# Kernel optimization log

Hardware: AMD Instinct MI355X
Metric: run time of the kernel (lower is better)

The kernel has to match this reference:

```python
import jax, jax.numpy as jnp
import numpy as np

B, N, IN_DIM, D, H, NC = 4, 1024, 8, 128, 8, 64
DK = D // H      # per-head key/value dim = 16
FF = 512         # hard-coded feedforward hidden
N_ENC = 6        # encoder layers


def _u(key, shape):
    s = 1.0 / np.sqrt(shape[-1])
    return jax.random.uniform(key, shape, jnp.float32, -s, s)


def setup_inputs() -> dict:
    key = jax.random.key(0)
    ks = jax.random.split(key, 24)
    inp = {}
    inp["node_inputs"] = jax.random.normal(ks[0], (B, N, IN_DIM), jnp.float32)
    inp["node_padding_mask"] = jnp.zeros((B, 1, N), jnp.int32)
    inp["edge_mask"] = jax.random.randint(ks[1], (B, N, N), 0, 2).astype(jnp.int32)
    inp["center_mask"] = jnp.zeros((B, 1, NC), jnp.int32)
    inp["center_index"] = jax.random.randint(ks[2], (B, 1, NC), 0, N)
    inp["target_index"] = jax.random.randint(ks[3], (B, 1, 1), 0, N)
    inp["current_index"] = jax.random.randint(ks[4], (B, 1, 1), 0, N)
    inp["edge_inputs"] = jax.random.randint(ks[5], (B, N, 20), 0, N)
    # params
    inp["init_W"] = _u(ks[6], (IN_DIM, D)); inp["init_b"] = jnp.zeros((D,), jnp.float32)
    inp["enc_wq"] = _u(ks[7], (N_ENC, H, D, DK))
    inp["enc_wk"] = _u(ks[8], (N_ENC, H, D, DK))
    inp["enc_wv"] = _u(ks[9], (N_ENC, H, D, DK))
    inp["enc_wo"] = _u(ks[10], (N_ENC, H, DK, D))
    inp["enc_ln1_g"] = jnp.ones((N_ENC, D), jnp.float32); inp["enc_ln1_b"] = jnp.zeros((N_ENC, D), jnp.float32)
    inp["enc_w1"] = _u(ks[11], (N_ENC, D, FF)); inp["enc_b1"] = jnp.zeros((N_ENC, FF), jnp.float32)
    inp["enc_w2"] = _u(ks[12], (N_ENC, FF, D)); inp["enc_b2"] = jnp.zeros((N_ENC, D), jnp.float32)
    inp["enc_ln2_g"] = jnp.ones((N_ENC, D), jnp.float32); inp["enc_ln2_b"] = jnp.zeros((N_ENC, D), jnp.float32)
    inp["dec_wq"] = _u(ks[13], (H, D, DK))
    inp["dec_wk"] = _u(ks[14], (H, D, DK))
    inp["dec_wv"] = _u(ks[15], (H, D, DK))
    inp["dec_wo"] = _u(ks[16], (H, DK, D))
    inp["dec_ln1_g"] = jnp.ones((D,), jnp.float32); inp["dec_ln1_b"] = jnp.zeros((D,), jnp.float32)
    inp["dec_w1"] = _u(ks[17], (D, FF)); inp["dec_b1"] = jnp.zeros((FF,), jnp.float32)
    inp["dec_w2"] = _u(ks[18], (FF, D)); inp["dec_b2"] = jnp.zeros((D,), jnp.float32)
    inp["dec_ln2_g"] = jnp.ones((D,), jnp.float32); inp["dec_ln2_b"] = jnp.zeros((D,), jnp.float32)
    inp["tgt_W"] = _u(ks[19], (2 * D, D)); inp["tgt_b"] = jnp.zeros((D,), jnp.float32)
    inp["ptr_wq"] = _u(ks[20], (D, D))
    inp["ptr_wk"] = _u(ks[21], (D, D))
    return inp


def _ln(x, g, b):
    m = jnp.mean(x, -1, keepdims=True)
    v = jnp.mean((x - m) ** 2, -1, keepdims=True)
    return (x - m) * jax.lax.rsqrt(v + 1e-5) * g + b


def _mha(q, k, v, wq, wk, wv, wo, mask):
    # per-head projections exactly as the torch module: [H, B, n, DK]
    Q = jnp.einsum('bqd,hde->hbqe', q, wq)
    K = jnp.einsum('bkd,hde->hbke', k, wk)
    V = jnp.einsum('bkd,hde->hbke', v, wv)
    U = jnp.einsum('hbqe,hbke->hbqk', Q, K) * (1.0 / np.sqrt(DK))
    if mask is not None:
        U = jnp.where(mask[None] > 0, -1e8, U)
    A = jax.nn.softmax(U, axis=-1)
    Hd = jnp.einsum('hbqk,hbke->hbqe', A, V)
    out = jnp.einsum('hbqe,hed->bqd', Hd, wo)
    return out, A


def _gather(x, idx):
    # x [B, N, D], idx [B, M, 1] -> [B, M, D]  (torch.gather with repeat)
    return jnp.take_along_axis(x, jnp.broadcast_to(idx, (x.shape[0], idx.shape[1], x.shape[2])), axis=1)


def reference(node_inputs, node_padding_mask, edge_mask, center_mask, center_index,
              target_index, current_index, edge_inputs,
              init_W, init_b,
              enc_wq, enc_wk, enc_wv, enc_wo, enc_ln1_g, enc_ln1_b,
              enc_w1, enc_b1, enc_w2, enc_b2, enc_ln2_g, enc_ln2_b,
              dec_wq, dec_wk, dec_wv, dec_wo, dec_ln1_g, dec_ln1_b,
              dec_w1, dec_b1, dec_w2, dec_b2, dec_ln2_g, dec_ln2_b,
              tgt_W, tgt_b, ptr_wq, ptr_wk):
    x = node_inputs @ init_W + init_b                      # initial_embedding
    enc_mask = edge_mask + node_padding_mask               # attn_mask + key_padding_mask, [B,N,N]
    for i in range(N_ENC):                                 # Encoder, 6 layers
        h = _ln(x, enc_ln1_g[i], enc_ln1_b[i])
        a, _ = _mha(h, h, h, enc_wq[i], enc_wk[i], enc_wv[i], enc_wo[i], enc_mask)
        h = a + x
        f = _ln(h, enc_ln2_g[i], enc_ln2_b[i])
        f = jax.nn.relu(f @ enc_w1[i] + enc_b1[i]) @ enc_w2[i] + enc_b2[i]
        x = f + h
    enh = x                                                # enhanced_node_feature [B,N,D]
    ci = jnp.transpose(center_index, (0, 2, 1))            # [B,NC,1]
    tgt_f = _gather(enh, target_index)                     # [B,1,D]
    cur_f = _gather(enh, current_index)                    # [B,1,D]
    cen_f = _gather(enh, ci)                               # [B,NC,D]
    # target_decoder (1 DecoderLayer; normalization1 applied to tgt AND memory)
    tgt_n = _ln(tgt_f, dec_ln1_g, dec_ln1_b)
    mem_n = _ln(enh, dec_ln1_g, dec_ln1_b)
    a, _ = _mha(tgt_n, mem_n, mem_n, dec_wq, dec_wk, dec_wv, dec_wo, node_padding_mask)
    h = a + tgt_f
    f = _ln(h, dec_ln2_g, dec_ln2_b)
    f = jax.nn.relu(f @ dec_w1 + dec_b1) @ dec_w2 + dec_b2
    enh_tgt = f + h                                        # [B,1,D]
    emb_tgt = jnp.concatenate([enh_tgt, tgt_f], -1) @ tgt_W + tgt_b
    # pointer1 (SingleHeadAttention, key_dim = D, tanh clipping 10)
    Q = emb_tgt @ ptr_wq                                   # [B,1,D]
    K = cen_f @ ptr_wk                                     # [B,NC,D]
    U = jnp.einsum('bqd,bkd->bqk', Q, K) * (1.0 / np.sqrt(D))
    U = 10.0 * jnp.tanh(U)
    U = jnp.where(center_mask == 1, -1e8, U)
    center_logp = jax.nn.log_softmax(U, axis=-1)[:, 0, :]  # [B,NC]
    idx = jnp.argmax(center_logp, axis=1)
    bidx = jnp.arange(B)
    selected_center_index = ci[bidx, idx, :]               # [B,1]
    selected_center_feature = cen_f[bidx, idx, :][:, None, :]  # [B,1,D]
    return (enh, cur_f, selected_center_index, selected_center_feature, center_logp, cen_f)
```

## Files before the change

kernel.cpp:

```cpp
#include <hip/hip_runtime.h>

constexpr int kB = 4, kN = 1024, kIn = 8, kD = 128, kH = 8, kNC = 64,
              kDK = 16, kFF = 512, kEnc = 6, kR = kB * kN;

__device__ __forceinline__ float wredsum(float v) {
  v += __shfl_xor(v, 1);  v += __shfl_xor(v, 2);  v += __shfl_xor(v, 4);
  v += __shfl_xor(v, 8);  v += __shfl_xor(v, 16); v += __shfl_xor(v, 32);
  return v;
}
__device__ __forceinline__ float wredmax(float v) {
  v = fmaxf(v, __shfl_xor(v, 1));  v = fmaxf(v, __shfl_xor(v, 2));
  v = fmaxf(v, __shfl_xor(v, 4));  v = fmaxf(v, __shfl_xor(v, 8));
  v = fmaxf(v, __shfl_xor(v, 16)); v = fmaxf(v, __shfl_xor(v, 32));
  return v;
}
__device__ __forceinline__ float red4(float v) {
  v += __shfl_xor(v, 1);  v += __shfl_xor(v, 2);
  return v;
}


__global__ __launch_bounds__(256) void repack_qkv(
    const float* __restrict__ wq, const float* __restrict__ wk,
    const float* __restrict__ wv, float* __restrict__ out, int layers) {
  int i = blockIdx.x * 256 + threadIdx.x;
  if (i >= layers * kD * kD) return;
  int l = i / (kD * kD);
  int rem = i - l * kD * kD;
  int d = rem >> 7;
  int c = rem & 127;
  int src = ((l * kH + (c >> 4)) * kD + d) * kDK + (c & 15);
  out[(size_t)(l * 3 + 0) * 16384 + rem] = wq[src];
  out[(size_t)(l * 3 + 1) * 16384 + rem] = wk[src];
  out[(size_t)(l * 3 + 2) * 16384 + rem] = wv[src];
}

__global__ __launch_bounds__(256) void pack_mask(
    const int* __restrict__ edge_mask, const int* __restrict__ pad_mask,
    unsigned long long* __restrict__ bits_t) {
  int row = blockIdx.x;
  int b = row / kN;
  int q = row % kN;
  int lane = threadIdx.x & 63;
  int wv = threadIdx.x >> 6;
  for (int c0 = wv; c0 < 16; c0 += 4) {
    int k = c0 * 64 + lane;
    int m = edge_mask[(size_t)row * kN + k] + pad_mask[b * kN + k];
    unsigned long long bal = __ballot(m > 0);
    if (lane == 0) bits_t[((size_t)b * 16 + c0) * kN + q] = bal;
  }
}

__global__ __launch_bounds__(256) void pack_pad(
    const int* __restrict__ pad_mask, unsigned long long* __restrict__ bits) {
  int b = blockIdx.x;
  int lane = threadIdx.x & 63;
  int wv = threadIdx.x >> 6;
  for (int c0 = wv; c0 < 16; c0 += 4) {
    int k = c0 * 64 + lane;
    unsigned long long bal = __ballot(pad_mask[b * kN + k] > 0);
    if (lane == 0) bits[b * 16 + c0] = bal;
  }
}

__global__ __launch_bounds__(256) void init_proj(
    const float* __restrict__ ni, const float* __restrict__ W,
    const float* __restrict__ bias, float* __restrict__ x) {
  int i = blockIdx.x * 256 + threadIdx.x;
  int r = i >> 7, c = i & 127;
  float acc = bias[c];
#pragma unroll
  for (int k = 0; k < kIn; k++) acc = fmaf(ni[r * kIn + k], W[k * kD + c], acc);
  x[i] = acc;
}

template <int K, int LN, int RELU, int MODE>
__global__ __launch_bounds__(256) void gtile4(
    const float* __restrict__ A, const float* __restrict__ Wg,
    const float* __restrict__ gamma, const float* __restrict__ beta,
    const float* __restrict__ bias, const float* __restrict__ resid,
    float* __restrict__ O0, float* __restrict__ O1, float* __restrict__ O2,
    int Cfull) {
  constexpr int NC = K / 32;
  __shared__ float As[16][K + 4];
  __shared__ float Ws[2][32][128];
  int r0 = blockIdx.x * 16;
  int y = blockIdx.y;
  const float* Wb;
  int wstride;
  if constexpr (MODE == 2) { Wb = Wg + (size_t)y * K * 128; wstride = 128; }
  else { Wb = Wg + (size_t)y * 128; wstride = Cfull; }

  if constexpr (LN) {
    static_assert(K == 128, "LN requires K==128");
    int w = threadIdx.x >> 6, lane = threadIdx.x & 63;
#pragma unroll
    for (int i = 0; i < 4; i++) {
      int rr = w * 4 + i;
      const float* xr = A + (size_t)(r0 + rr) * 128;
      float2 v = *(const float2*)(xr + lane * 2);
      float mean = wredsum(v.x + v.y) * (1.0f / 128.f);
      float dx = v.x - mean, dy = v.y - mean;
      float var = wredsum(dx * dx + dy * dy) * (1.0f / 128.f);
      float rstd = rsqrtf(var + 1e-5f);
      int c = lane * 2;
      As[rr][c] = dx * rstd * gamma[c] + beta[c];
      As[rr][c + 1] = dy * rstd * gamma[c + 1] + beta[c + 1];
    }
  } else if constexpr (MODE == 3) {
    static_assert(K == 128, "merge stage requires K==128");
    for (int f = threadIdx.x; f < 16 * 32; f += 256) {
      int row = f >> 5, c4i = f & 31;
      int r = r0 + row;
      int bb = r >> 10, q = r & 1023;
      int hh = c4i >> 2, e4 = (c4i & 3) * 4;
      const float* p0 = A + ((size_t)((bb * kH + hh) * kN + q)) * 20;
      const size_t stride = (size_t)32 * kN * 20;
      float m0 = p0[16], l0 = p0[17];
      float m1 = p0[stride + 16], l1 = p0[stride + 17];
      float m2 = p0[2 * stride + 16], l2 = p0[2 * stride + 17];
      float m3 = p0[3 * stride + 16], l3 = p0[3 * stride + 17];
      float ms = fmaxf(fmaxf(m0, m1), fmaxf(m2, m3));
      float f0 = __expf(m0 - ms), f1 = __expf(m1 - ms);
      float f2 = __expf(m2 - ms), f3 = __expf(m3 - ms);
      float inv = 1.0f / (f0 * l0 + f1 * l1 + f2 * l2 + f3 * l3);
      float4 a0 = *(const float4*)(p0 + e4);
      float4 a1 = *(const float4*)(p0 + stride + e4);
      float4 a2 = *(const float4*)(p0 + 2 * stride + e4);
      float4 a3 = *(const float4*)(p0 + 3 * stride + e4);
      float4 o;
      o.x = (f0 * a0.x + f1 * a1.x + f2 * a2.x + f3 * a3.x) * inv;
      o.y = (f0 * a0.y + f1 * a1.y + f2 * a2.y + f3 * a3.y) * inv;
      o.z = (f0 * a0.z + f1 * a1.z + f2 * a2.z + f3 * a3.z) * inv;
      o.w = (f0 * a0.w + f1 * a1.w + f2 * a2.w + f3 * a3.w) * inv;
      *(float4*)&As[row][c4i * 4] = o;
    }
  } else {
    constexpr int NF4 = K / 4;
    for (int f = threadIdx.x; f < 16 * NF4; f += 256) {
      int row = f / NF4, c4i = f % NF4;
      *(float4*)&As[row][c4i * 4] =
          *(const float4*)(A + (size_t)(r0 + row) * K + c4i * 4);
    }
  }

  int wrow = threadIdx.x >> 5;
  int wc4 = threadIdx.x & 31;
  float4 wreg[4];
  auto loadW = [&](int kc) {
    const float* Wr = Wb + (size_t)(kc * 32 + wrow) * wstride + wc4 * 4;
#pragma unroll
    for (int j = 0; j < 4; j++)
      wreg[j] = *(const float4*)(Wr + (size_t)8 * j * wstride);
  };
  auto writeW = [&](int buf) {
#pragma unroll
    for (int j = 0; j < 4; j++)
      *(float4*)&Ws[buf][wrow + 8 * j][wc4 * 4] = wreg[j];
  };

  loadW(0);
  writeW(0);

  int c4 = (threadIdx.x & 31) * 4;
  int rg = threadIdx.x >> 5;
  float acc[2][4] = {};
  for (int kc = 0; kc < NC; kc++) {
    if (kc + 1 < NC) loadW(kc + 1);
    __syncthreads();
#pragma unroll
    for (int k4 = 0; k4 < 8; k4++) {
      float4 a0 = *(const float4*)&As[rg * 2][kc * 32 + k4 * 4];
      float4 a1 = *(const float4*)&As[rg * 2 + 1][kc * 32 + k4 * 4];
#pragma unroll
      for (int m = 0; m < 4; m++) {
        float4 wv = *(const float4*)&Ws[kc & 1][k4 * 4 + m][c4];
        float av0 = ((const float*)&a0)[m];
        float av1 = ((const float*)&a1)[m];
        acc[0][0] = fmaf(av0, wv.x, acc[0][0]);
        acc[0][1] = fmaf(av0, wv.y, acc[0][1]);
        acc[0][2] = fmaf(av0, wv.z, acc[0][2]);
        acc[0][3] = fmaf(av0, wv.w, acc[0][3]);
        acc[1][0] = fmaf(av1, wv.x, acc[1][0]);
        acc[1][1] = fmaf(av1, wv.y, acc[1][1]);
        acc[1][2] = fmaf(av1, wv.z, acc[1][2]);
        acc[1][3] = fmaf(av1, wv.w, acc[1][3]);
      }
    }
    if (kc + 1 < NC) writeW((kc + 1) & 1);
  }

#pragma unroll
  for (int rr = 0; rr < 2; rr++) {
    int r = r0 + rg * 2 + rr;
    if constexpr (MODE == 2) {
#pragma unroll
      for (int j = 0; j < 4; j++) {
        int c = c4 + j;
        float v = acc[rr][j];
        int hh = c >> 4, e = c & 15;
        int bb = r >> 10, n = r & 1023;
        float* P = (y == 0) ? O0 : (y == 1) ? O1 : O2;
        P[(((size_t)(bb * kH + hh)) * kN + n) * kDK + e] = v;
      }
    } else {
      int colg = y * 128 + c4;
      float4 v = make_float4(acc[rr][0], acc[rr][1], acc[rr][2], acc[rr][3]);
      if (bias) {
        float4 bv = *(const float4*)(bias + colg);
        v.x += bv.x; v.y += bv.y; v.z += bv.z; v.w += bv.w;
      }
      if (resid) {
        float4 rv = *(const float4*)(resid + (size_t)r * Cfull + colg);
        v.x += rv.x; v.y += rv.y; v.z += rv.z; v.w += rv.w;
      }
      if (RELU) {
        v.x = fmaxf(v.x, 0.f); v.y = fmaxf(v.y, 0.f);
        v.z = fmaxf(v.z, 0.f); v.w = fmaxf(v.w, 0.f);
      }
      *(float4*)(O0 + (size_t)r * Cfull + colg) = v;
    }
  }
}

__global__ __launch_bounds__(512) void attn_part(
    const float* __restrict__ Q, const float* __restrict__ K,
    const float* __restrict__ V, const unsigned long long* __restrict__ bits_t,
    float* __restrict__ part) {
  __shared__ float KV[2][8][32][20];
  int bh = blockIdx.x, qt = blockIdx.y, ks = blockIdx.z;
  int b = bh >> 3;
  int w = threadIdx.x >> 6, lane = threadIdx.x & 63;
  int qbase = qt * 256 + lane;
  float4 qr[4][4];
#pragma unroll
  for (int i = 0; i < 4; i++) {
    const float4* qp =
        (const float4*)(Q + ((size_t)bh * kN + qbase + i * 64) * kDK);
    qr[i][0] = qp[0]; qr[i][1] = qp[1]; qr[i][2] = qp[2]; qr[i][3] = qp[3];
  }
  int tile = ks * 4 + (w >> 1);
  int bitoff = (w & 1) * 32;
  unsigned long long mb[4];
#pragma unroll
  for (int i = 0; i < 4; i++)
    mb[i] = bits_t[((size_t)b * 16 + tile) * kN + qbase + i * 64];

  float mx[4], lsum[4], acc[4][16];
#pragma unroll
  for (int i = 0; i < 4; i++) {
    mx[i] = -3.0e38f; lsum[i] = 0.f;
#pragma unroll
    for (int e = 0; e < 16; e++) acc[i][e] = 0.f;
  }

  int kb = ks * 256 + w * 32;
  int srow = lane >> 1, shalf = (lane & 1) * 8;
  {
    const float* kr = K + ((size_t)bh * kN + kb + srow) * kDK + shalf;
    const float* vr = V + ((size_t)bh * kN + kb + srow) * kDK + shalf;
    *(float4*)&KV[0][w][srow][shalf] = *(const float4*)kr;
    *(float4*)&KV[0][w][srow][shalf + 4] = *(const float4*)(kr + 4);
    *(float4*)&KV[1][w][srow][shalf] = *(const float4*)vr;
    *(float4*)&KV[1][w][srow][shalf + 4] = *(const float4*)(vr + 4);
  }
#pragma unroll 2
  for (int k2 = 0; k2 < 32; k2++) {
    const float4* kr4 = (const float4*)&KV[0][w][k2][0];
    float4 k0 = kr4[0], k1 = kr4[1], k2v = kr4[2], k3 = kr4[3];
    const float4* vr4 = (const float4*)&KV[1][w][k2][0];
    float4 v0 = vr4[0], v1 = vr4[1], v2 = vr4[2], v3 = vr4[3];
    int kbit = bitoff + k2;
#pragma unroll
    for (int i = 0; i < 4; i++) {
      float s = qr[i][0].x * k0.x + qr[i][0].y * k0.y + qr[i][0].z * k0.z +
                qr[i][0].w * k0.w + qr[i][1].x * k1.x + qr[i][1].y * k1.y +
                qr[i][1].z * k1.z + qr[i][1].w * k1.w + qr[i][2].x * k2v.x +
                qr[i][2].y * k2v.y + qr[i][2].z * k2v.z + qr[i][2].w * k2v.w +
                qr[i][3].x * k3.x + qr[i][3].y * k3.y + qr[i][3].z * k3.z +
                qr[i][3].w * k3.w;
      s *= 0.25f;
      if ((mb[i] >> kbit) & 1ull) s = -1e8f;
      float d = s - mx[i];
      if (d > 8.f) {
        float sc = __expf(-d);
        lsum[i] *= sc;
#pragma unroll
        for (int e = 0; e < 16; e++) acc[i][e] *= sc;
        mx[i] = s; d = 0.f;
      }
      float p = __expf(d);
      lsum[i] += p;
      acc[i][0] = fmaf(p, v0.x, acc[i][0]);
      acc[i][1] = fmaf(p, v0.y, acc[i][1]);
      acc[i][2] = fmaf(p, v0.z, acc[i][2]);
      acc[i][3] = fmaf(p, v0.w, acc[i][3]);
      acc[i][4] = fmaf(p, v1.x, acc[i][4]);
      acc[i][5] = fmaf(p, v1.y, acc[i][5]);
      acc[i][6] = fmaf(p, v1.z, acc[i][6]);
      acc[i][7] = fmaf(p, v1.w, acc[i][7]);
      acc[i][8] = fmaf(p, v2.x, acc[i][8]);
      acc[i][9] = fmaf(p, v2.y, acc[i][9]);
      acc[i][10] = fmaf(p, v2.z, acc[i][10]);
      acc[i][11] = fmaf(p, v2.w, acc[i][11]);
      acc[i][12] = fmaf(p, v3.x, acc[i][12]);
      acc[i][13] = fmaf(p, v3.y, acc[i][13]);
      acc[i][14] = fmaf(p, v3.z, acc[i][14]);
      acc[i][15] = fmaf(p, v3.w, acc[i][15]);
    }
  }
  __syncthreads();
  float* scratch = &KV[0][0][0][0];
  for (int i = 0; i < 4; i++) {
    float* dst = scratch + (size_t)(w * 64 + lane) * 20;
#pragma unroll
    for (int e = 0; e < 16; e++) dst[e] = acc[i][e];
    dst[16] = mx[i];
    dst[17] = lsum[i];
    __syncthreads();
    if (w == 0) {
      float mv[8];
#pragma unroll
      for (int p = 0; p < 8; p++) mv[p] = scratch[(p * 64 + lane) * 20 + 16];
      float mstar = mv[0];
#pragma unroll
      for (int p = 1; p < 8; p++) mstar = fmaxf(mstar, mv[p]);
      float f[8];
      float L = 0.f;
#pragma unroll
      for (int p = 0; p < 8; p++) {
        f[p] = __expf(mv[p] - mstar);
        L += f[p] * scratch[(p * 64 + lane) * 20 + 17];
      }
      int q = qt * 256 + i * 64 + lane;
      float* op = part + ((size_t)(ks * 32 + bh) * kN + q) * 20;
#pragma unroll
      for (int e = 0; e < 16; e++) {
        float a = 0.f;
#pragma unroll
        for (int p = 0; p < 8; p++)
          a += f[p] * scratch[(p * 64 + lane) * 20 + e];
        op[e] = a;
      }
      op[16] = mstar;
      op[17] = L;
    }
    __syncthreads();
  }
}


__global__ __launch_bounds__(256) void dec_prep(
    const float* __restrict__ enh, const int* __restrict__ tgt_idx,
    const int* __restrict__ cur_idx, const int* __restrict__ cen_idx,
    const float* __restrict__ Wq,
    const float* __restrict__ ln1_g, const float* __restrict__ ln1_b,
    const float* __restrict__ dec_wk,
    float* __restrict__ out_curf, float* __restrict__ out_cenf,
    float* __restrict__ tgtf_ws, float* __restrict__ qk_ws) {
  __shared__ float tgtf_s[128], tgtn[128], qd[128];
  int b = blockIdx.x, t = threadIdx.x;
  int lane = t & 63, w = t >> 6;
  int ti = tgt_idx[b], cui = cur_idx[b];
  if (t < 128) {
    float tf = enh[((size_t)b * kN + ti) * kD + t];
    tgtf_s[t] = tf;
    tgtf_ws[b * kD + t] = tf;
    out_curf[b * kD + t] = enh[((size_t)b * kN + cui) * kD + t];
  }
  for (int i = t; i < kNC * kD; i += 256) {
    int c = i >> 7, e = i & 127;
    out_cenf[((size_t)b * kNC + c) * kD + e] =
        enh[((size_t)b * kN + cen_idx[b * kNC + c]) * kD + e];
  }
  __syncthreads();
  if (w == 0) {
    float vx = tgtf_s[lane * 2], vy = tgtf_s[lane * 2 + 1];
    float mean = wredsum(vx + vy) * (1.0f / 128.f);
    float dx = vx - mean, dy = vy - mean;
    float var = wredsum(dx * dx + dy * dy) * (1.0f / 128.f);
    float rstd = rsqrtf(var + 1e-5f);
    tgtn[lane * 2] = dx * rstd * ln1_g[lane * 2] + ln1_b[lane * 2];
    tgtn[lane * 2 + 1] = dy * rstd * ln1_g[lane * 2 + 1] + ln1_b[lane * 2 + 1];
  }
  __syncthreads();
  if (t < 128) {
    float a = 0.f;
#pragma unroll 8
    for (int k = 0; k < 128; k++) a = fmaf(tgtn[k], Wq[k * 128 + t], a);
    qd[t] = a;
  }
  __syncthreads();
  int h = t >> 5, d0 = (t & 31) * 4;
#pragma unroll
  for (int j = 0; j < 4; j++) {
    int d = d0 + j;
    const float4* wp = (const float4*)(dec_wk + (((size_t)h * 128 + d) << 4));
    float a = 0.f;
#pragma unroll
    for (int r = 0; r < 4; r++) {
      float4 wv = wp[r];
      a += wv.x * qd[h * 16 + r * 4] + wv.y * qd[h * 16 + r * 4 + 1] +
           wv.z * qd[h * 16 + r * 4 + 2] + wv.w * qd[h * 16 + r * 4 + 3];
    }
    qk_ws[b * 1024 + h * 128 + d] = 0.25f * a;
  }
}

__global__ __launch_bounds__(256) void dec_score(
    const float* __restrict__ enh, const float* __restrict__ ln_g,
    const float* __restrict__ ln_b, const float* __restrict__ qk_ws,
    const unsigned long long* __restrict__ padbits,
    float* __restrict__ ln_ws, float* __restrict__ scores) {
  __shared__ float qs[8][128];
  int b = blockIdx.x, nt = blockIdx.y, t = threadIdx.x;
  for (int i = t; i < 1024; i += 256) ((float*)qs)[i] = qk_ws[b * 1024 + i];
  __syncthreads();
  int w = t >> 6, lane = t & 63, ri = lane >> 2, q4 = lane & 3;
  int n = nt * 64 + w * 16 + ri;
  const float* row = enh + ((size_t)b * kN + n) * kD;
  float4 xv[8];
#pragma unroll
  for (int j = 0; j < 8; j++) xv[j] = *(const float4*)(row + j * 16 + q4 * 4);
  float s1 = 0.f;
#pragma unroll
  for (int j = 0; j < 8; j++) s1 += xv[j].x + xv[j].y + xv[j].z + xv[j].w;
  s1 = red4(s1);
  float mean = s1 * (1.0f / 128.f);
  float s2 = 0.f;
#pragma unroll
  for (int j = 0; j < 8; j++) {
    xv[j].x -= mean; xv[j].y -= mean; xv[j].z -= mean; xv[j].w -= mean;
    s2 += xv[j].x * xv[j].x + xv[j].y * xv[j].y + xv[j].z * xv[j].z +
          xv[j].w * xv[j].w;
  }
  s2 = red4(s2);
  float rstd = rsqrtf(s2 * (1.0f / 128.f) + 1e-5f);
#pragma unroll
  for (int j = 0; j < 8; j++) {
    int d0 = j * 16 + q4 * 4;
    float4 g = *(const float4*)(ln_g + d0);
    float4 be = *(const float4*)(ln_b + d0);
    xv[j].x = xv[j].x * rstd * g.x + be.x;
    xv[j].y = xv[j].y * rstd * g.y + be.y;
    xv[j].z = xv[j].z * rstd * g.z + be.z;
    xv[j].w = xv[j].w * rstd * g.w + be.w;
    *(float4*)(ln_ws + ((size_t)b * kN + n) * kD + d0) = xv[j];
  }
  bool mk = (padbits[b * 16 + (n >> 6)] >> (n & 63)) & 1ull;
#pragma unroll
  for (int h = 0; h < 8; h++) {
    float p = 0.f;
#pragma unroll
    for (int j = 0; j < 8; j++) {
      float4 qv = *(const float4*)&qs[h][j * 16 + q4 * 4];
      p += xv[j].x * qv.x + xv[j].y * qv.y + xv[j].z * qv.z + xv[j].w * qv.w;
    }
    p = red4(p);
    if (q4 == 0) scores[((size_t)b * 8 + h) * 1024 + n] = mk ? -1e8f : p;
  }
}

__global__ __launch_bounds__(256) void dec_softmax(
    const float* __restrict__ scores, float* __restrict__ ml) {
  int b = blockIdx.x, t = threadIdx.x, w = t >> 6, lane = t & 63;
  for (int hi = 0; hi < 2; hi++) {
    int h = w + hi * 4;
    const float* sr = scores + ((size_t)b * 8 + h) * 1024;
    float v[16];
    float m = -3.0e38f;
#pragma unroll
    for (int i = 0; i < 16; i++) { v[i] = sr[i * 64 + lane]; m = fmaxf(m, v[i]); }
    m = wredmax(m);
    float l = 0.f;
#pragma unroll
    for (int i = 0; i < 16; i++) l += __expf(v[i] - m);
    l = wredsum(l);
    if (lane == 0) { ml[(b * 8 + h) * 2] = m; ml[(b * 8 + h) * 2 + 1] = l; }
  }
}

__global__ __launch_bounds__(256) void dec_attnsum(
    const float* __restrict__ ln_ws, const float* __restrict__ scores,
    const float* __restrict__ ml, float* __restrict__ partial) {
  __shared__ float lns[64][128];
  __shared__ float ps[8][64];
  int b = blockIdx.x, nt = blockIdx.y, t = threadIdx.x;
  for (int i = t; i < 64 * 32; i += 256) {
    int nn = i >> 5, c4 = i & 31;
    *(float4*)&lns[nn][c4 * 4] =
        *(const float4*)(ln_ws + ((size_t)b * kN + nt * 64 + nn) * kD + c4 * 4);
  }
  for (int i = t; i < 512; i += 256) {
    int h = i >> 6, nn = i & 63;
    float m = ml[(b * 8 + h) * 2], l = ml[(b * 8 + h) * 2 + 1];
    ps[h][nn] =
        __expf(scores[((size_t)b * 8 + h) * 1024 + nt * 64 + nn] - m) / l;
  }
  __syncthreads();
  int h = t >> 5, d0 = (t & 31) * 4;
  float4 acc = make_float4(0.f, 0.f, 0.f, 0.f);
  for (int nn = 0; nn < 64; nn++) {
    float p = ps[h][nn];
    float4 lv = *(const float4*)&lns[nn][d0];
    acc.x = fmaf(p, lv.x, acc.x); acc.y = fmaf(p, lv.y, acc.y);
    acc.z = fmaf(p, lv.z, acc.z); acc.w = fmaf(p, lv.w, acc.w);
  }
  *(float4*)(partial + ((size_t)(b * 16 + nt) * 8 + h) * 128 + d0) = acc;
}

__global__ __launch_bounds__(1024) void dec_tail(
    const float* __restrict__ partial, const float* __restrict__ dec_wv,
    const float* __restrict__ dwo, const float* __restrict__ tgtf_ws,
    const float* __restrict__ cenf_g, const float* __restrict__ Kp,
    const int* __restrict__ cen_idx, const int* __restrict__ center_mask,
    const float* __restrict__ ln2_g, const float* __restrict__ ln2_b,
    const float* __restrict__ w1, const float* __restrict__ b1,
    const float* __restrict__ w2, const float* __restrict__ b2,
    const float* __restrict__ tgt_W, const float* __restrict__ tgt_b,
    const float* __restrict__ ptr_wq,
    float* __restrict__ out_selidx, float* __restrict__ out_selfeat,
    float* __restrict__ out_logp) {
  __shared__ float wsum[8][132];
  __shared__ float red[8][132];
  __shared__ float red2[2][520];
  __shared__ float red16[16][68];
  __shared__ float tgtf[128], hdd[128], dechs[128], decfs[128], dects[512],
                   embs[128], qps[128];
  __shared__ int bi_s;
  int b = blockIdx.x, t = threadIdx.x;
  int c = t & 127, p = t >> 7;
  int lane = t & 63, w = t >> 6;

  {
    float a = 0.f;
#pragma unroll
    for (int tt = 0; tt < 16; tt++)
      a += partial[((size_t)(b * 16 + tt) * 8 + p) * 128 + c];
    wsum[p][c] = a;
    if (t < 128) tgtf[t] = tgtf_ws[b * kD + t];
  }
  __syncthreads();

  {
    int h = c >> 4, e = c & 15;
    float a = 0.f;
#pragma unroll
    for (int i = 0; i < 16; i++) {
      int d = p * 16 + i;
      a = fmaf(wsum[h][d], dec_wv[((size_t)h * 128 + d) * 16 + e], a);
    }
    red[p][c] = a;
  }
  __syncthreads();
  if (t < 128) {
    float a = 0.f;
#pragma unroll
    for (int q = 0; q < 8; q++) a += red[q][t];
    hdd[t] = a;
  }
  __syncthreads();

  {
    float a = 0.f;
#pragma unroll
    for (int i = 0; i < 16; i++) {
      int k = p * 16 + i;
      a = fmaf(hdd[k], dwo[k * 128 + c], a);
    }
    red[p][c] = a;
  }
  __syncthreads();
  if (t < 128) {
    float a = 0.f;
#pragma unroll
    for (int q = 0; q < 8; q++) a += red[q][t];
    dechs[t] = a + tgtf[t];
  }
  __syncthreads();

  if (w == 0) {
    float vx = dechs[lane * 2], vy = dechs[lane * 2 + 1];
    float mean = wredsum(vx + vy) * (1.0f / 128.f);
    float dx = vx - mean, dy = vy - mean;
    float var = wredsum(dx * dx + dy * dy) * (1.0f / 128.f);
    float rstd = rsqrtf(var + 1e-5f);
    decfs[lane * 2] = dx * rstd * ln2_g[lane * 2] + ln2_b[lane * 2];
    decfs[lane * 2 + 1] = dy * rstd * ln2_g[lane * 2 + 1] + ln2_b[lane * 2 + 1];
  }
  __syncthreads();

  {
    int c5 = t & 511, p2 = t >> 9;
    float a = 0.f;
#pragma unroll 8
    for (int i = 0; i < 64; i++) {
      int k = p2 * 64 + i;
      a = fmaf(decfs[k], w1[k * 512 + c5], a);
    }
    red2[p2][c5] = a;
  }
  __syncthreads();
  if (t < 512) dects[t] = fmaxf(red2[0][t] + red2[1][t] + b1[t], 0.f);
  __syncthreads();

  {
    float a = 0.f;
#pragma unroll 8
    for (int i = 0; i < 64; i++) {
      int k = p * 64 + i;
      a = fmaf(dects[k], w2[k * 128 + c], a);
    }
    red[p][c] = a;
  }
  __syncthreads();
  if (t < 128) {
    float a = 0.f;
#pragma unroll
    for (int q = 0; q < 8; q++) a += red[q][t];
    decfs[t] = a + b2[t] + dechs[t];
  }
  __syncthreads();

  {
    float a = 0.f;
#pragma unroll
    for (int i = 0; i < 32; i++) {
      int k = p * 32 + i;
      float vkk = (k < 128) ? decfs[k] : tgtf[k - 128];
      a = fmaf(vkk, tgt_W[k * 128 + c], a);
    }
    red[p][c] = a;
  }
  __syncthreads();
  if (t < 128) {
    float a = 0.f;
#pragma unroll
    for (int q = 0; q < 8; q++) a += red[q][t];
    embs[t] = a + tgt_b[t];
  }
  __syncthreads();

  {
    float a = 0.f;
#pragma unroll
    for (int i = 0; i < 16; i++) {
      int k = p * 16 + i;
      a = fmaf(embs[k], ptr_wq[k * 128 + c], a);
    }
    red[p][c] = a;
  }
  __syncthreads();
  if (t < 128) {
    float a = 0.f;
#pragma unroll
    for (int q = 0; q < 8; q++) a += red[q][t];
    qps[t] = a;
  }
  __syncthreads();

  {
    int cen = t & 63, p16 = t >> 6;
    float a = 0.f;
#pragma unroll
    for (int i = 0; i < 8; i++) {
      int k = p16 * 8 + i;
      a = fmaf(qps[k], Kp[((size_t)(b * kNC + cen)) * kD + k], a);
    }
    red16[p16][cen] = a;
  }
  __syncthreads();
  if (w == 0) {
    float u = 0.f;
#pragma unroll
    for (int q = 0; q < 16; q++) u += red16[q][lane];
    u *= 0.08838834764831845f;
    u = 10.0f * tanhf(u);
    if (center_mask[b * kNC + lane] == 1) u = -1e8f;
    float m = wredmax(u);
    float ex = __expf(u - m);
    float sum = wredsum(ex);
    out_logp[b * kNC + lane] = u - m - logf(sum);
    float bm = u; int bi = lane;
#pragma unroll
    for (int o = 32; o; o >>= 1) {
      float om = __shfl_xor(bm, o);
      int oi = __shfl_xor(bi, o);
      if (om > bm || (om == bm && oi < bi)) { bm = om; bi = oi; }
    }
    if (lane == 0) {
      out_selidx[b] = (float)cen_idx[b * kNC + bi];
      bi_s = bi;
    }
  }
  __syncthreads();
  if (t < 128)
    out_selfeat[b * kD + t] = cenf_g[((size_t)(b * kNC + bi_s)) * kD + t];
}


extern "C" void kernel_launch(void* const* d_in, const int* in_sizes, int n_in,
                              void* d_out, int out_size, void* d_ws,
                              size_t ws_size, hipStream_t stream) {
  (void)in_sizes; (void)n_in; (void)out_size; (void)ws_size;
  const float* node_inputs = (const float*)d_in[0];
  const int* pad_mask = (const int*)d_in[1];
  const int* edge_mask = (const int*)d_in[2];
  const int* center_mask = (const int*)d_in[3];
  const int* center_index = (const int*)d_in[4];
  const int* target_index = (const int*)d_in[5];
  const int* current_index = (const int*)d_in[6];
  const float* init_W = (const float*)d_in[8];
  const float* init_b = (const float*)d_in[9];
  const float* enc_wq = (const float*)d_in[10];
  const float* enc_wk = (const float*)d_in[11];
  const float* enc_wv = (const float*)d_in[12];
  const float* enc_wo = (const float*)d_in[13];
  const float* enc_ln1_g = (const float*)d_in[14];
  const float* enc_ln1_b = (const float*)d_in[15];
  const float* enc_w1 = (const float*)d_in[16];
  const float* enc_b1 = (const float*)d_in[17];
  const float* enc_w2 = (const float*)d_in[18];
  const float* enc_b2 = (const float*)d_in[19];
  const float* enc_ln2_g = (const float*)d_in[20];
  const float* enc_ln2_b = (const float*)d_in[21];
  const float* dec_wq = (const float*)d_in[22];
  const float* dec_wk = (const float*)d_in[23];
  const float* dec_wv = (const float*)d_in[24];
  const float* dec_wo = (const float*)d_in[25];
  const float* dec_ln1_g = (const float*)d_in[26];
  const float* dec_ln1_b = (const float*)d_in[27];
  const float* dec_w1 = (const float*)d_in[28];
  const float* dec_b1 = (const float*)d_in[29];
  const float* dec_w2 = (const float*)d_in[30];
  const float* dec_b2 = (const float*)d_in[31];
  const float* dec_ln2_g = (const float*)d_in[32];
  const float* dec_ln2_b = (const float*)d_in[33];
  const float* tgt_W = (const float*)d_in[34];
  const float* tgt_b = (const float*)d_in[35];
  const float* ptr_wq = (const float*)d_in[36];
  const float* ptr_wk = (const float*)d_in[37];

  float* out_enh = (float*)d_out;
  float* out_curf = out_enh + kB * kN * kD;
  float* out_selidx = out_curf + kB * kD;
  float* out_selfeat = out_selidx + kB;
  float* out_logp = out_selfeat + kB * kD;
  float* out_cenf = out_logp + kB * kNC;

  char* wsp = (char*)d_ws;
  size_t off = 0;
  auto alloc = [&](size_t n) {
    char* p = wsp + off;
    off = (off + n + 255) & ~(size_t)255;
    return p;
  };
  float* x   = (float*)alloc(kR * kD * 4);
  float* h2  = (float*)alloc(kR * kD * 4);
  float* Qb  = (float*)alloc(kR * kD * 4);
  float* Kb  = (float*)alloc(kR * kD * 4);
  float* Vb  = (float*)alloc(kR * kD * 4);
  float* tb  = (float*)alloc(kR * kFF * 4);
  unsigned long long* bits_t  = (unsigned long long*)alloc(kR * 16 * 8);
  unsigned long long* padbits = (unsigned long long*)alloc(kB * 16 * 8);
  float* ewqkv = (float*)alloc(kEnc * 3 * kD * kD * 4);
  float* dqkvW = (float*)alloc(3 * kD * kD * 4);
  float* ln_ws = (float*)alloc(kR * kD * 4);
  float* scores_ws = (float*)alloc(kB * kH * kN * 4);
  float* ml_ws = (float*)alloc(kB * kH * 2 * 4);
  float* partial_ws = (float*)alloc(kB * 16 * kH * kD * 4);
  float* qk_ws = (float*)alloc(kB * kH * kD * 4);
  float* tgtf_ws = (float*)alloc(kB * kD * 4);
  float* Kp_ws = (float*)alloc(kB * kNC * kD * 4);
  float* apart_ws = (float*)alloc((size_t)4 * 32 * kN * 20 * 4);

  repack_qkv<<<(kEnc * kD * kD + 255) / 256, 256, 0, stream>>>(
      enc_wq, enc_wk, enc_wv, ewqkv, kEnc);
  repack_qkv<<<(kD * kD + 255) / 256, 256, 0, stream>>>(
      dec_wq, dec_wk, dec_wv, dqkvW, 1);
  pack_mask<<<kB * kN, 256, 0, stream>>>(edge_mask, pad_mask, bits_t);
  pack_pad<<<kB, 256, 0, stream>>>(pad_mask, padbits);
  init_proj<<<kR * kD / 256, 256, 0, stream>>>(node_inputs, init_W, init_b, x);

  for (int l = 0; l < kEnc; l++) {
    const float* wo_l = enc_wo + (size_t)l * kH * kDK * kD;
    gtile4<128, 1, 0, 2><<<dim3(kR / 16, 3), 256, 0, stream>>>(
        x, ewqkv + (size_t)l * 3 * kD * kD, enc_ln1_g + l * kD,
        enc_ln1_b + l * kD, nullptr, nullptr, Qb, Kb, Vb, kD);
    attn_part<<<dim3(kB * kH, kN / 256, 4), 512, 0, stream>>>(Qb, Kb, Vb,
                                                              bits_t, apart_ws);
    gtile4<128, 0, 0, 3><<<dim3(kR / 16, 1), 256, 0, stream>>>(
        apart_ws, wo_l, nullptr, nullptr, nullptr, x, h2, nullptr, nullptr, kD);
    gtile4<128, 1, 1, 0><<<dim3(kR / 16, kFF / 128), 256, 0, stream>>>(
        h2, enc_w1 + (size_t)l * kD * kFF, enc_ln2_g + l * kD,
        enc_ln2_b + l * kD, enc_b1 + l * kFF, nullptr, tb, nullptr, nullptr, kFF);
    float* xout = (l == kEnc - 1) ? out_enh : x;
    gtile4<512, 0, 0, 0><<<dim3(kR / 16, 1), 256, 0, stream>>>(
        tb, enc_w2 + (size_t)l * kFF * kD, nullptr, nullptr, enc_b2 + l * kD,
        h2, xout, nullptr, nullptr, kD);
  }

  dec_prep<<<kB, 256, 0, stream>>>(out_enh, target_index, current_index,
                                   center_index, dqkvW, dec_ln1_g, dec_ln1_b,
                                   dec_wk, out_curf, out_cenf, tgtf_ws, qk_ws);
  gtile4<128, 0, 0, 0><<<dim3(kB * kNC / 16, 1), 256, 0, stream>>>(
      out_cenf, ptr_wk, nullptr, nullptr, nullptr, nullptr, Kp_ws, nullptr,
      nullptr, kD);
  dec_score<<<dim3(kB, 16), 256, 0, stream>>>(out_enh, dec_ln1_g, dec_ln1_b,
                                              qk_ws, padbits, ln_ws, scores_ws);
  dec_softmax<<<kB, 256, 0, stream>>>(scores_ws, ml_ws);
  dec_attnsum<<<dim3(kB, 16), 256, 0, stream>>>(ln_ws, scores_ws, ml_ws,
                                                partial_ws);
  dec_tail<<<kB, 1024, 0, stream>>>(
      partial_ws, dec_wv, dec_wo, tgtf_ws, out_cenf, Kp_ws, center_index,
      center_mask, dec_ln2_g, dec_ln2_b, dec_w1, dec_b1, dec_w2, dec_b2,
      tgt_W, tgt_b, ptr_wq, out_selidx, out_selfeat, out_logp);
}
```

Baseline: 849.0 us.

## Parallelize attention partial merge across warps and shrink GEMM k-chunks

The attention split-merge epilogue previously had only warp 0 combine eight per-warp partials serially from padded shared scratch. Now every warp rescales its own accumulator, writes it swizzled into shared memory, and one warp per query row-group sums the partials with float4 reads. The generic GEMM tile kernel gains a row-tile template (TR) and 16-wide k-chunks, so the output-projection merge stage can launch twice as many blocks with 8 rows each. A separate specialized gtile4 is kept for K=512 and the pointer projection. The cost is more syncthreads in the merge and less reuse per weight tile in the smaller tiles.

```diff
diff --git a/kernel.cpp b/kernel.cpp
--- a/kernel.cpp
+++ b/kernel.cpp
@@ -74,17 +74,18 @@
   x[i] = acc;
 }
 
-template <int K, int LN, int RELU, int MODE>
-__global__ __launch_bounds__(256) void gtile4(
+template <int K, int TR, int LN, int RELU, int MODE>
+__global__ __launch_bounds__(256) void gtile5(
     const float* __restrict__ A, const float* __restrict__ Wg,
     const float* __restrict__ gamma, const float* __restrict__ beta,
     const float* __restrict__ bias, const float* __restrict__ resid,
     float* __restrict__ O0, float* __restrict__ O1, float* __restrict__ O2,
     int Cfull) {
-  constexpr int NC = K / 32;
-  __shared__ float As[16][K + 4];
-  __shared__ float Ws[2][32][128];
-  int r0 = blockIdx.x * 16;
+  constexpr int NC = K / 16;
+  constexpr int RPT = TR / 8;
+  __shared__ float As[TR][K + 4];
+  __shared__ float Ws[2][16][128];
+  int r0 = blockIdx.x * TR;
   int y = blockIdx.y;
   const float* Wb;
   int wstride;
@@ -92,7 +93,7 @@
   else { Wb = Wg + (size_t)y * 128; wstride = Cfull; }
 
   if constexpr (LN) {
-    static_assert(K == 128, "LN requires K==128");
+    static_assert(K == 128 && TR == 16, "LN requires K==128, TR==16");
     int w = threadIdx.x >> 6, lane = threadIdx.x & 63;
 #pragma unroll
     for (int i = 0; i < 4; i++) {
@@ -109,7 +110,7 @@
     }
   } else if constexpr (MODE == 3) {
     static_assert(K == 128, "merge stage requires K==128");
-    for (int f = threadIdx.x; f < 16 * 32; f += 256) {
+    for (int f = threadIdx.x; f < TR * 32; f += 256) {
       int row = f >> 5, c4i = f & 31;
       int r = r0 + row;
       int bb = r >> 10, q = r & 1023;
@@ -137,7 +138,7 @@
     }
   } else {
     constexpr int NF4 = K / 4;
-    for (int f = threadIdx.x; f < 16 * NF4; f += 256) {
+    for (int f = threadIdx.x; f < TR * NF4; f += 256) {
       int row = f / NF4, c4i = f % NF4;
       *(float4*)&As[row][c4i * 4] =
           *(const float4*)(A + (size_t)(r0 + row) * K + c4i * 4);
@@ -146,17 +147,15 @@
 
   int wrow = threadIdx.x >> 5;
   int wc4 = threadIdx.x & 31;
-  float4 wreg[4];
+  float4 wreg[2];
   auto loadW = [&](int kc) {
-    const float* Wr = Wb + (size_t)(kc * 32 + wrow) * wstride + wc4 * 4;
-#pragma unroll
-    for (int j = 0; j < 4; j++)
-      wreg[j] = *(const float4*)(Wr + (size_t)8 * j * wstride);
+    const float* Wr = Wb + (size_t)(kc * 16 + wrow) * wstride + wc4 * 4;
+    wreg[0] = *(const float4*)Wr;
+    wreg[1] = *(const float4*)(Wr + (size_t)8 * wstride);
   };
   auto writeW = [&](int buf) {
-#pragma unroll
-    for (int j = 0; j < 4; j++)
-      *(float4*)&Ws[buf][wrow + 8 * j][wc4 * 4] = wreg[j];
+    *(float4*)&Ws[buf][wrow][wc4 * 4] = wreg[0];
+    *(float4*)&Ws[buf][wrow + 8][wc4 * 4] = wreg[1];
   };
 
   loadW(0);
@@ -164,35 +163,35 @@
 
   int c4 = (threadIdx.x & 31) * 4;
   int rg = threadIdx.x >> 5;
-  float acc[2][4] = {};
+  float acc[RPT][4] = {};
   for (int kc = 0; kc < NC; kc++) {
     if (kc + 1 < NC) loadW(kc + 1);
     __syncthreads();
 #pragma unroll
-    for (int k4 = 0; k4 < 8; k4++) {
-      float4 a0 = *(const float4*)&As[rg * 2][kc * 32 + k4 * 4];
-      float4 a1 = *(const float4*)&As[rg * 2 + 1][kc * 32 + k4 * 4];
+    for (int k4 = 0; k4 < 4; k4++) {
+      float4 a[RPT];
+#pragma unroll
+      for (int rr = 0; rr < RPT; rr++)
+        a[rr] = *(const float4*)&As[rg * RPT + rr][kc * 16 + k4 * 4];
 #pragma unroll
       for (int m = 0; m < 4; m++) {
         float4 wv = *(const float4*)&Ws[kc & 1][k4 * 4 + m][c4];
-        float av0 = ((const float*)&a0)[m];
-        float av1 = ((const float*)&a1)[m];
-        acc[0][0] = fmaf(av0, wv.x, acc[0][0]);
-        acc[0][1] = fmaf(av0, wv.y, acc[0][1]);
-        acc[0][2] = fmaf(av0, wv.z, acc[0][2]);
-        acc[0][3] = fmaf(av0, wv.w, acc[0][3]);
-        acc[1][0] = fmaf(av1, wv.x, acc[1][0]);
-        acc[1][1] = fmaf(av1, wv.y, acc[1][1]);
-        acc[1][2] = fmaf(av1, wv.z, acc[1][2]);
-        acc[1][3] = fmaf(av1, wv.w, acc[1][3]);
+#pragma unroll
+        for (int rr = 0; rr < RPT; rr++) {
+          float av = ((const float*)&a[rr])[m];
+          acc[rr][0] = fmaf(av, wv.x, acc[rr][0]);
+          acc[rr][1] = fmaf(av, wv.y, acc[rr][1]);
+          acc[rr][2] = fmaf(av, wv.z, acc[rr][2]);
+          acc[rr][3] = fmaf(av, wv.w, acc[rr][3]);
+        }
       }
     }
     if (kc + 1 < NC) writeW((kc + 1) & 1);
   }
 
 #pragma unroll
-  for (int rr = 0; rr < 2; rr++) {
-    int r = r0 + rg * 2 + rr;
+  for (int rr = 0; rr < RPT; rr++) {
+    int r = r0 + rg * RPT + rr;
     if constexpr (MODE == 2) {
 #pragma unroll
       for (int j = 0; j < 4; j++) {
@@ -223,11 +222,98 @@
   }
 }
 
-__global__ __launch_bounds__(512) void attn_part(
+template <int K, int RELU>
+__global__ __launch_bounds__(256) void gtile4(
+    const float* __restrict__ A, const float* __restrict__ Wg,
+    const float* __restrict__ bias, const float* __restrict__ resid,
+    float* __restrict__ O0, int Cfull) {
+  constexpr int NC = K / 32;
+  __shared__ float As[16][K + 4];
+  __shared__ float Ws[2][32][128];
+  int r0 = blockIdx.x * 16;
+  int y = blockIdx.y;
+  const float* Wb = Wg + (size_t)y * 128;
+  int wstride = Cfull;
+
+  constexpr int NF4 = K / 4;
+  for (int f = threadIdx.x; f < 16 * NF4; f += 256) {
+    int row = f / NF4, c4i = f % NF4;
+    *(float4*)&As[row][c4i * 4] =
+        *(const float4*)(A + (size_t)(r0 + row) * K + c4i * 4);
+  }
+
+  int wrow = threadIdx.x >> 5;
+  int wc4 = threadIdx.x & 31;
+  float4 wreg[4];
+  auto loadW = [&](int kc) {
+    const float* Wr = Wb + (size_t)(kc * 32 + wrow) * wstride + wc4 * 4;
+#pragma unroll
+    for (int j = 0; j < 4; j++)
+      wreg[j] = *(const float4*)(Wr + (size_t)8 * j * wstride);
+  };
+  auto writeW = [&](int buf) {
+#pragma unroll
+    for (int j = 0; j < 4; j++)
+      *(float4*)&Ws[buf][wrow + 8 * j][wc4 * 4] = wreg[j];
+  };
+
+  loadW(0);
+  writeW(0);
+
+  int c4 = (threadIdx.x & 31) * 4;
+  int rg = threadIdx.x >> 5;
+  float acc[2][4] = {};
+  for (int kc = 0; kc < NC; kc++) {
+    if (kc + 1 < NC) loadW(kc + 1);
+    __syncthreads();
+#pragma unroll
+    for (int k4 = 0; k4 < 8; k4++) {
+      float4 a0 = *(const float4*)&As[rg * 2][kc * 32 + k4 * 4];
+      float4 a1 = *(const float4*)&As[rg * 2 + 1][kc * 32 + k4 * 4];
+#pragma unroll
+      for (int m = 0; m < 4; m++) {
+        float4 wv = *(const float4*)&Ws[kc & 1][k4 * 4 + m][c4];
+        float av0 = ((const float*)&a0)[m];
+        float av1 = ((const float*)&a1)[m];
+        acc[0][0] = fmaf(av0, wv.x, acc[0][0]);
+        acc[0][1] = fmaf(av0, wv.y, acc[0][1]);
+        acc[0][2] = fmaf(av0, wv.z, acc[0][2]);
+        acc[0][3] = fmaf(av0, wv.w, acc[0][3]);
+        acc[1][0] = fmaf(av1, wv.x, acc[1][0]);
+        acc[1][1] = fmaf(av1, wv.y, acc[1][1]);
+        acc[1][2] = fmaf(av1, wv.z, acc[1][2]);
+        acc[1][3] = fmaf(av1, wv.w, acc[1][3]);
+      }
+    }
+    if (kc + 1 < NC) writeW((kc + 1) & 1);
+  }
+
+#pragma unroll
+  for (int rr = 0; rr < 2; rr++) {
+    int r = r0 + rg * 2 + rr;
+    int colg = y * 128 + c4;
+    float4 v = make_float4(acc[rr][0], acc[rr][1], acc[rr][2], acc[rr][3]);
+    if (bias) {
+      float4 bv = *(const float4*)(bias + colg);
+      v.x += bv.x; v.y += bv.y; v.z += bv.z; v.w += bv.w;
+    }
+    if (resid) {
+      float4 rv = *(const float4*)(resid + (size_t)r * Cfull + colg);
+      v.x += rv.x; v.y += rv.y; v.z += rv.z; v.w += rv.w;
+    }
+    if (RELU) {
+      v.x = fmaxf(v.x, 0.f); v.y = fmaxf(v.y, 0.f);
+      v.z = fmaxf(v.z, 0.f); v.w = fmaxf(v.w, 0.f);
+    }
+    *(float4*)(O0 + (size_t)r * Cfull + colg) = v;
+  }
+}
+
+__global__ __launch_bounds__(512) void attn_part2(
     const float* __restrict__ Q, const float* __restrict__ K,
     const float* __restrict__ V, const unsigned long long* __restrict__ bits_t,
     float* __restrict__ part) {
-  __shared__ float KV[2][8][32][20];
+  __shared__ float KV[2][8][32][16];
   int bh = blockIdx.x, qt = blockIdx.y, ks = blockIdx.z;
   int b = bh >> 3;
   int w = threadIdx.x >> 6, lane = threadIdx.x & 63;
@@ -309,38 +395,48 @@
       acc[i][15] = fmaf(p, v3.w, acc[i][15]);
     }
   }
-  __syncthreads();
-  float* scratch = &KV[0][0][0][0];
+
+  __syncthreads();
+  float* sc = &KV[0][0][0][0];
+  int row = w * 64 + lane;
+  int swz = ((lane >> 1) & 3) << 2;
   for (int i = 0; i < 4; i++) {
-    float* dst = scratch + (size_t)(w * 64 + lane) * 20;
-#pragma unroll
-    for (int e = 0; e < 16; e++) dst[e] = acc[i][e];
-    dst[16] = mx[i];
-    dst[17] = lsum[i];
+    sc[row * 2] = mx[i];
+    sc[row * 2 + 1] = lsum[i];
     __syncthreads();
-    if (w == 0) {
-      float mv[8];
-#pragma unroll
-      for (int p = 0; p < 8; p++) mv[p] = scratch[(p * 64 + lane) * 20 + 16];
-      float mstar = mv[0];
-#pragma unroll
-      for (int p = 1; p < 8; p++) mstar = fmaxf(mstar, mv[p]);
-      float f[8];
-      float L = 0.f;
-#pragma unroll
-      for (int p = 0; p < 8; p++) {
-        f[p] = __expf(mv[p] - mstar);
-        L += f[p] * scratch[(p * 64 + lane) * 20 + 17];
-      }
-      int q = qt * 256 + i * 64 + lane;
-      float* op = part + ((size_t)(ks * 32 + bh) * kN + q) * 20;
-#pragma unroll
-      for (int e = 0; e < 16; e++) {
-        float a = 0.f;
-#pragma unroll
-        for (int p = 0; p < 8; p++)
-          a += f[p] * scratch[(p * 64 + lane) * 20 + e];
-        op[e] = a;
+    float mv[8], lv[8];
+#pragma unroll
+    for (int p = 0; p < 8; p++) {
+      mv[p] = sc[(p * 64 + lane) * 2];
+      lv[p] = sc[(p * 64 + lane) * 2 + 1];
+    }
+    float mstar = mv[0];
+#pragma unroll
+    for (int p = 1; p < 8; p++) mstar = fmaxf(mstar, mv[p]);
+    float fw = __expf(mv[w] - mstar);
+    float L = 0.f;
+#pragma unroll
+    for (int p = 0; p < 8; p++) L += __expf(mv[p] - mstar) * lv[p];
+    __syncthreads();
+#pragma unroll
+    for (int eg = 0; eg < 4; eg++) {
+      float4 v = make_float4(acc[i][eg * 4] * fw, acc[i][eg * 4 + 1] * fw,
+                             acc[i][eg * 4 + 2] * fw, acc[i][eg * 4 + 3] * fw);
+      *(float4*)&sc[row * 16 + ((eg * 4) ^ swz)] = v;
+    }
+    __syncthreads();
+    if (w == i) {
+      float* op = part + ((size_t)(ks * 32 + bh) * kN + qt * 256 + i * 64 +
+                          lane) * 20;
+#pragma unroll
+      for (int eg = 0; eg < 4; eg++) {
+        float4 s = make_float4(0.f, 0.f, 0.f, 0.f);
+#pragma unroll
+        for (int p = 0; p < 8; p++) {
+          float4 t = *(const float4*)&sc[(p * 64 + lane) * 16 + ((eg * 4) ^ swz)];
+          s.x += t.x; s.y += t.y; s.z += t.z; s.w += t.w;
+        }
+        *(float4*)(op + eg * 4) = s;
       }
       op[16] = mstar;
       op[17] = L;
@@ -784,28 +880,26 @@
 
   for (int l = 0; l < kEnc; l++) {
     const float* wo_l = enc_wo + (size_t)l * kH * kDK * kD;
-    gtile4<128, 1, 0, 2><<<dim3(kR / 16, 3), 256, 0, stream>>>(
+    gtile5<128, 16, 1, 0, 2><<<dim3(kR / 16, 3), 256, 0, stream>>>(
         x, ewqkv + (size_t)l * 3 * kD * kD, enc_ln1_g + l * kD,
         enc_ln1_b + l * kD, nullptr, nullptr, Qb, Kb, Vb, kD);
-    attn_part<<<dim3(kB * kH, kN / 256, 4), 512, 0, stream>>>(Qb, Kb, Vb,
-                                                              bits_t, apart_ws);
-    gtile4<128, 0, 0, 3><<<dim3(kR / 16, 1), 256, 0, stream>>>(
+    attn_part2<<<dim3(kB * kH, kN / 256, 4), 512, 0, stream>>>(Qb, Kb, Vb,
+                                                               bits_t, apart_ws);
+    gtile5<128, 8, 0, 0, 3><<<dim3(kR / 8, 1), 256, 0, stream>>>(
         apart_ws, wo_l, nullptr, nullptr, nullptr, x, h2, nullptr, nullptr, kD);
-    gtile4<128, 1, 1, 0><<<dim3(kR / 16, kFF / 128), 256, 0, stream>>>(
+    gtile5<128, 16, 1, 1, 0><<<dim3(kR / 16, kFF / 128), 256, 0, stream>>>(
         h2, enc_w1 + (size_t)l * kD * kFF, enc_ln2_g + l * kD,
         enc_ln2_b + l * kD, enc_b1 + l * kFF, nullptr, tb, nullptr, nullptr, kFF);
     float* xout = (l == kEnc - 1) ? out_enh : x;
-    gtile4<512, 0, 0, 0><<<dim3(kR / 16, 1), 256, 0, stream>>>(
-        tb, enc_w2 + (size_t)l * kFF * kD, nullptr, nullptr, enc_b2 + l * kD,
-        h2, xout, nullptr, nullptr, kD);
+    gtile4<512, 0><<<dim3(kR / 16, 1), 256, 0, stream>>>(
+        tb, enc_w2 + (size_t)l * kFF * kD, enc_b2 + l * kD, h2, xout, kD);
   }
 
   dec_prep<<<kB, 256, 0, stream>>>(out_enh, target_index, current_index,
                                    center_index, dqkvW, dec_ln1_g, dec_ln1_b,
                                    dec_wk, out_curf, out_cenf, tgtf_ws, qk_ws);
-  gtile4<128, 0, 0, 0><<<dim3(kB * kNC / 16, 1), 256, 0, stream>>>(
-      out_cenf, ptr_wk, nullptr, nullptr, nullptr, nullptr, Kp_ws, nullptr,
-      nullptr, kD);
+  gtile4<128, 0><<<dim3(kB * kNC / 16, 1), 256, 0, stream>>>(
+      out_cenf, ptr_wk, nullptr, nullptr, Kp_ws, kD);
   dec_score<<<dim3(kB, 16), 256, 0, stream>>>(out_enh, dec_ln1_g, dec_ln1_b,
                                               qk_ws, padbits, ln_ws, scores_ws);
   dec_softmax<<<kB, 256, 0, stream>>>(scores_ws, ml_ws);
```

Result: slower. 872.3 us (+2.7%).
